# Optimization experiments

Hardware: AMD Instinct MI355X
Metric: run time of the kernel (lower is better)

The kernel has to match this reference:

```python
import jax, jax.numpy as jnp
import numpy as np

D_MODEL, N_HEADS, D_LLM = 1024, 16, 4096
D_KEYS = D_MODEL // N_HEADS  # 64


def setup_inputs() -> dict:
    key = jax.random.key(0)
    ks = jax.random.split(key, 11)
    s = lambda fan_in: 1.0 / np.sqrt(fan_in)
    inp = {
        "target_embedding": jax.random.normal(ks[0], (4, 2048, D_MODEL), jnp.float32),
        "source_embedding": jax.random.normal(ks[1], (4, 1024, D_LLM), jnp.float32),
        "value_embedding": jax.random.normal(ks[2], (4, 1024, D_LLM), jnp.float32),
        "Wq": jax.random.uniform(ks[3], (D_MODEL, D_KEYS * N_HEADS), jnp.float32, -s(D_MODEL), s(D_MODEL)),
        "bq": jax.random.uniform(ks[4], (D_KEYS * N_HEADS,), jnp.float32, -s(D_MODEL), s(D_MODEL)),
        "Wk": jax.random.uniform(ks[5], (D_LLM, D_KEYS * N_HEADS), jnp.float32, -s(D_LLM), s(D_LLM)),
        "bk": jax.random.uniform(ks[6], (D_KEYS * N_HEADS,), jnp.float32, -s(D_LLM), s(D_LLM)),
        "Wv": jax.random.uniform(ks[7], (D_LLM, D_KEYS * N_HEADS), jnp.float32, -s(D_LLM), s(D_LLM)),
        "bv": jax.random.uniform(ks[8], (D_KEYS * N_HEADS,), jnp.float32, -s(D_LLM), s(D_LLM)),
        "Wo": jax.random.uniform(ks[9], (D_KEYS * N_HEADS, D_MODEL), jnp.float32, -s(D_KEYS * N_HEADS), s(D_KEYS * N_HEADS)),
        "bo": jax.random.uniform(ks[10], (D_MODEL,), jnp.float32, -s(D_KEYS * N_HEADS), s(D_KEYS * N_HEADS)),
    }
    return inp


def reference(target_embedding, source_embedding, value_embedding,
              Wq, bq, Wk, bk, Wv, bv, Wo, bo):
    B, L, _ = target_embedding.shape
    _, S, _ = source_embedding.shape
    H, E = N_HEADS, D_KEYS
    q = (target_embedding @ Wq + bq).reshape(B, L, H, E)
    k = (source_embedding @ Wk + bk).reshape(B, S, H, E)
    v = (value_embedding @ Wv + bv).reshape(B, S, H, E)
    scale = 1.0 / np.sqrt(E)
    scores = jnp.einsum('blhe,bshe->bhls', q, k)  # [B,H,L,S]
    A = jax.nn.softmax(scale * scores, axis=-1)   # dropout = identity (eval mode)
    out = jnp.einsum('bhls,bshe->blhe', A, v).reshape(B, L, H * E)
    return out @ Wo + bo
```

## Files before the change

kernel.cpp:

```cpp
#include <hip/hip_runtime.h>
#include <hip/hip_bf16.h>

using bf16 = __hip_bfloat16;
typedef __attribute__((ext_vector_type(8))) short short8;
typedef __attribute__((ext_vector_type(4))) float f32x4;

static constexpr int Bc = 4, Lc = 2048, Sc = 1024;
static constexpr int DModel = 1024;

__device__ __forceinline__ void gload16(const void* g, void* l) {
  __builtin_amdgcn_global_load_lds((const __attribute__((address_space(1))) void*)g,
                                   (__attribute__((address_space(3))) void*)l,
                                   16, 0, 0);
}

__device__ __forceinline__ void wait_vm8()  { asm volatile("s_waitcnt vmcnt(8)" ::: "memory"); }
__device__ __forceinline__ void wait_vm4()  { asm volatile("s_waitcnt vmcnt(4)" ::: "memory"); }
__device__ __forceinline__ void wait_vm0()  { asm volatile("s_waitcnt vmcnt(0)" ::: "memory"); }
__device__ __forceinline__ void barrier_raw() { asm volatile("s_barrier" ::: "memory"); }

__global__ void cvt3(const float* __restrict__ a, bf16* __restrict__ ao, long na4,
                     const float* __restrict__ b, bf16* __restrict__ bo, long nb4,
                     const float* __restrict__ c, bf16* __restrict__ co, long nc4) {
  long total = na4 + nb4 + nc4;
  long stride = (long)gridDim.x * blockDim.x;
  for (long i = (long)blockIdx.x * blockDim.x + threadIdx.x; i < total; i += stride) {
    const float* src; bf16* dst; long j;
    if (i < na4)            { src = a; dst = ao; j = i; }
    else if (i < na4 + nb4) { src = b; dst = bo; j = i - na4; }
    else                    { src = c; dst = co; j = i - na4 - nb4; }
    float4 v = reinterpret_cast<const float4*>(src)[j];
    alignas(8) bf16 t[4] = {__float2bfloat16(v.x), __float2bfloat16(v.y),
                            __float2bfloat16(v.z), __float2bfloat16(v.w)};
    reinterpret_cast<ushort4*>(dst)[j] = *reinterpret_cast<const ushort4*>(t);
  }
}

__global__ __launch_bounds__(256) void transpose_cvt_w(const float* __restrict__ Wq, bf16* __restrict__ WqT,
                                                       const float* __restrict__ Wk, bf16* __restrict__ WkT,
                                                       const float* __restrict__ Wv, bf16* __restrict__ WvT,
                                                       const float* __restrict__ Wo, bf16* __restrict__ WoT) {
  __shared__ bf16 tile[32][33];
  int bid = blockIdx.x;
  const float* in; bf16* out; int R, l;
  if (bid < 1024)      { in = Wq; out = WqT; R = 1024; l = bid; }
  else if (bid < 5120) { in = Wk; out = WkT; R = 4096; l = bid - 1024; }
  else if (bid < 9216) { in = Wv; out = WvT; R = 4096; l = bid - 5120; }
  else                 { in = Wo; out = WoT; R = 1024; l = bid - 9216; }
  const int C = 1024;
  int bx = l & 31, by = l >> 5;
  int tx = threadIdx.x & 31, ty = threadIdx.x >> 5;
  int r0 = by * 32, c0 = bx * 32;
#pragma unroll
  for (int i = 0; i < 32; i += 8)
    tile[ty + i][tx] = __float2bfloat16(in[(long)(r0 + ty + i) * C + c0 + tx]);
  __syncthreads();
#pragma unroll
  for (int i = 0; i < 32; i += 8)
    out[(long)(c0 + ty + i) * R + r0 + tx] = tile[tx][ty + i];
}

__device__ __forceinline__ void gemm_core(const bf16* __restrict__ A, const bf16* __restrict__ Bt,
                                          const float* __restrict__ bias,
                                          bf16* __restrict__ Cb, float* __restrict__ Cf,
                                          bf16* __restrict__ Cvt,
                                          int N, int K, int bx, int by,
                                          bf16* As, bf16* Bs) {
  const int tid = threadIdx.x;
  const int lane = tid & 63, g = lane >> 4, lm = lane & 15;
  const int wid = tid >> 6, wr = wid >> 1, wc = wid & 1;
  const long brow = (long)by * 128, bcol = (long)bx * 128;

  const bf16* asrc[4];
  const bf16* bsrc[4];
  int dsto[4];
#pragma unroll
  for (int t = 0; t < 4; ++t) {
    int sl = tid + t * 256;
    int row = sl >> 3;
    int kg = (sl & 7) ^ (row & 7);
    asrc[t] = A + (brow + row) * (long)K + kg * 8;
    bsrc[t] = Bt + (bcol + row) * (long)K + kg * 8;
    dsto[t] = sl * 16;
  }

  f32x4 zero = {0.f, 0.f, 0.f, 0.f};
  f32x4 acc[4][4];
#pragma unroll
  for (int i = 0; i < 4; ++i)
#pragma unroll
    for (int j = 0; j < 4; ++j) acc[i][j] = zero;

  char* Asc = (char*)As;
  char* Bsc = (char*)Bs;

#pragma unroll
  for (int t = 0; t < 4; ++t) {
    gload16(asrc[t], Asc + dsto[t]);
    gload16(bsrc[t], Bsc + dsto[t]);
    asrc[t] += 64; bsrc[t] += 64;
  }

  const int nt = K >> 6;
  for (int i = 0; i < nt; ++i) {
    const int cur = i & 1;
    if (i + 1 < nt) {
      const int nxt = cur ^ 1;
#pragma unroll
      for (int t = 0; t < 4; ++t) {
        gload16(asrc[t], Asc + nxt * 16384 + dsto[t]);
        gload16(bsrc[t], Bsc + nxt * 16384 + dsto[t]);
        asrc[t] += 64; bsrc[t] += 64;
      }
      wait_vm8();
    } else {
      wait_vm0();
    }
    barrier_raw();

    const char* Ab = Asc + cur * 16384;
    const char* Bb = Bsc + cur * 16384;
    __builtin_amdgcn_s_setprio(1);
#pragma unroll
    for (int ks = 0; ks < 2; ++ks) {
      short8 af[4], bfv[4];
#pragma unroll
      for (int mi = 0; mi < 4; ++mi) {
        int m = wr * 64 + mi * 16 + lm;
        af[mi] = *reinterpret_cast<const short8*>(
            Ab + ((m * 128 + ks * 64 + g * 16) ^ ((m & 7) << 4)));
      }
#pragma unroll
      for (int ni = 0; ni < 4; ++ni) {
        int n = wc * 64 + ni * 16 + lm;
        bfv[ni] = *reinterpret_cast<const short8*>(
            Bb + ((n * 128 + ks * 64 + g * 16) ^ ((n & 7) << 4)));
      }
#pragma unroll
      for (int mi = 0; mi < 4; ++mi)
#pragma unroll
        for (int ni = 0; ni < 4; ++ni)
          acc[mi][ni] = __builtin_amdgcn_mfma_f32_16x16x32_bf16(af[mi], bfv[ni], acc[mi][ni], 0, 0, 0);
    }
    __builtin_amdgcn_s_setprio(0);
    barrier_raw();
  }

#pragma unroll
  for (int ni = 0; ni < 4; ++ni) {
    long n = bcol + wc * 64 + ni * 16 + lm;
    float bv = bias ? bias[n] : 0.f;
#pragma unroll
    for (int mi = 0; mi < 4; ++mi) {
      long m0 = brow + wr * 64 + mi * 16 + g * 4;
      if (Cvt) {
        long b = m0 >> 10, s0 = m0 & 1023;
        alignas(8) bf16 t4[4];
#pragma unroll
        for (int r = 0; r < 4; ++r) t4[r] = __float2bfloat16(acc[mi][ni][r] + bv);
        *reinterpret_cast<ushort4*>(Cvt + ((b << 10) + n) * 1024 + s0) =
            *reinterpret_cast<const ushort4*>(t4);
      } else {
#pragma unroll
        for (int r = 0; r < 4; ++r) {
          float o = acc[mi][ni][r] + bv;
          if (Cb) Cb[(m0 + r) * N + n] = __float2bfloat16(o);
          else    Cf[(m0 + r) * N + n] = o;
        }
      }
    }
  }
}

__global__ __launch_bounds__(256) void gemm_bt(const bf16* __restrict__ A,
                                               const bf16* __restrict__ Bt,
                                               const float* __restrict__ bias,
                                               bf16* __restrict__ Cb,
                                               float* __restrict__ Cf,
                                               int N, int K) {
  __shared__ bf16 As[2 * 128 * 64];
  __shared__ bf16 Bs[2 * 128 * 64];
  int bid = blockIdx.x;
  int g = (bid & 7) * (gridDim.x >> 3) + (bid >> 3);
  gemm_core(A, Bt, bias, Cb, Cf, nullptr, N, K, g & 7, g >> 3, As, Bs);
}

__global__ __launch_bounds__(256) void gemm_qkv(
    const bf16* __restrict__ Ak, const bf16* __restrict__ Bk, const float* __restrict__ bk_, bf16* __restrict__ Ck, int Kk, int nbk,
    const bf16* __restrict__ Av, const bf16* __restrict__ Bv_, const float* __restrict__ bv_, bf16* __restrict__ CvT, int Kv, int nbv,
    const bf16* __restrict__ Aq, const bf16* __restrict__ Bq_, const float* __restrict__ bq_, bf16* __restrict__ Cq, int Kq) {
  __shared__ bf16 As[2 * 128 * 64];
  __shared__ bf16 Bs[2 * 128 * 64];
  int bid = blockIdx.x;
  const bf16 *A, *Bt; const float* bias; bf16 *C = nullptr, *Cvt = nullptr; int K, l, nb;
  if (bid < nbk)            { A = Ak; Bt = Bk;  bias = bk_; C = Ck;    K = Kk; l = bid;             nb = nbk; }
  else if (bid < nbk + nbv) { A = Av; Bt = Bv_; bias = bv_; Cvt = CvT; K = Kv; l = bid - nbk;       nb = nbv; }
  else                      { A = Aq; Bt = Bq_; bias = bq_; C = Cq;   K = Kq; l = bid - nbk - nbv; nb = gridDim.x - nbk - nbv; }
  int g = (l & 7) * (nb >> 3) + (l >> 3);
  gemm_core(A, Bt, bias, C, nullptr, Cvt, 1024, K, g & 7, g >> 3, As, Bs);
}

__global__ __launch_bounds__(256) void attn_fused(const bf16* __restrict__ q,
                                                  const bf16* __restrict__ k,
                                                  const bf16* __restrict__ vT,
                                                  bf16* __restrict__ o) {
  constexpr float C2 = 0.18033688011112042f;
  constexpr float THR = 6.0f;
  __shared__ bf16 Kl[2][64 * 64];
  __shared__ bf16 Vl[2][64 * 64];
  __shared__ bf16 Pl[4][16 * 64];
  const int tid = threadIdx.x;
  const int lane = tid & 63, g = lane >> 4, lm = lane & 15;
  const int wid = tid >> 6;
  int bid = blockIdx.x;
  int gl = (bid & 7) * 256 + (bid >> 3);
  const int qt = gl & 31, bh = gl >> 5;
  const int b = bh >> 4, h = bh & 15;
  const int qbase = qt * 64 + wid * 16;

  const bf16* qrow = q + (long)(b * Lc + qbase + lm) * DModel + h * 64;
  short8 qa0 = *reinterpret_cast<const short8*>(qrow + g * 8);
  short8 qa1 = *reinterpret_cast<const short8*>(qrow + 32 + g * 8);
#pragma unroll
  for (int j = 0; j < 8; ++j) {
    union { ushort u; bf16 h; } cv;
    cv.u = (ushort)qa0[j];
    bf16 s0 = __float2bfloat16(__bfloat162float(cv.h) * C2);
    qa0[j] = (short)*reinterpret_cast<ushort*>(&s0);
    cv.u = (ushort)qa1[j];
    bf16 s1 = __float2bfloat16(__bfloat162float(cv.h) * C2);
    qa1[j] = (short)*reinterpret_cast<ushort*>(&s1);
  }

  const bf16* kbase = k + (long)b * Sc * DModel + h * 64;
  const bf16* vbase = vT + ((long)b * DModel + h * 64) * Sc;

  const bf16* ksrc[2];
  const bf16* vsrc[2];
  int dsto[2];
#pragma unroll
  for (int t = 0; t < 2; ++t) {
    int sl = tid + t * 256;
    int row = sl >> 3;
    int cg = (sl & 7) ^ (row & 7);
    ksrc[t] = kbase + (long)row * DModel + cg * 8;
    vsrc[t] = vbase + (long)row * Sc + cg * 8;
    dsto[t] = sl * 16;
  }

  f32x4 zero = {0.f, 0.f, 0.f, 0.f};
  f32x4 accO[4];
#pragma unroll
  for (int i = 0; i < 4; ++i) accO[i] = zero;
  f32x4 accL = zero;
  float mst[4] = {-1e30f, -1e30f, -1e30f, -1e30f};

  short8 vones;
#pragma unroll
  for (int j = 0; j < 8; ++j) vones[j] = (short)0x3F80;

  char* Klc = (char*)Kl;
  char* Vlc = (char*)Vl;
  char* Plc = (char*)Pl + wid * (16 * 64 * 2);

#pragma unroll
  for (int t = 0; t < 2; ++t) {
    gload16(ksrc[t], Klc + dsto[t]);
    gload16(vsrc[t], Vlc + dsto[t]);
    ksrc[t] += 64 * DModel; vsrc[t] += 64;
  }

  for (int j = 0; j < Sc / 64; ++j) {
    const int cur = j & 1;
    if (j + 1 < Sc / 64) {
      const int nxt = cur ^ 1;
#pragma unroll
      for (int t = 0; t < 2; ++t) {
        gload16(ksrc[t], Klc + nxt * 8192 + dsto[t]);
        gload16(vsrc[t], Vlc + nxt * 8192 + dsto[t]);
        ksrc[t] += 64 * DModel; vsrc[t] += 64;
      }
      wait_vm4();
    } else {
      wait_vm0();
    }
    barrier_raw();

    const char* Kb = Klc + cur * 8192;
    const char* Vb = Vlc + cur * 8192;

    f32x4 scv[4];
    __builtin_amdgcn_s_setprio(1);
#pragma unroll
    for (int st = 0; st < 4; ++st) {
      int s = st * 16 + lm;
      int sw = (s & 7) << 4;
      short8 kb0 = *reinterpret_cast<const short8*>(Kb + ((s * 128 + g * 16) ^ sw));
      short8 kb1 = *reinterpret_cast<const short8*>(Kb + ((s * 128 + 64 + g * 16) ^ sw));
      f32x4 z = zero;
      z = __builtin_amdgcn_mfma_f32_16x16x32_bf16(qa0, kb0, z, 0, 0, 0);
      z = __builtin_amdgcn_mfma_f32_16x16x32_bf16(qa1, kb1, z, 0, 0, 0);
      scv[st] = z;
    }
    __builtin_amdgcn_s_setprio(0);

    float pmax[4];
#pragma unroll
    for (int r = 0; r < 4; ++r)
      pmax[r] = fmaxf(fmaxf(scv[0][r], scv[1][r]), fmaxf(scv[2][r], scv[3][r]));
    int need = 0;
#pragma unroll
    for (int r = 0; r < 4; ++r) need |= (pmax[r] > mst[r] + THR) ? 1 : 0;
    if (__any(need)) {
#pragma unroll
      for (int r = 0; r < 4; ++r) {
        float mx = pmax[r];
        mx = fmaxf(mx, __shfl_xor(mx, 1));
        mx = fmaxf(mx, __shfl_xor(mx, 2));
        mx = fmaxf(mx, __shfl_xor(mx, 4));
        mx = fmaxf(mx, __shfl_xor(mx, 8));
        float mnew = fmaxf(mst[r], mx);
        float corr = __builtin_amdgcn_exp2f(mst[r] - mnew);
        mst[r] = mnew;
        accL[r] *= corr;
#pragma unroll
        for (int et = 0; et < 4; ++et) accO[et][r] *= corr;
      }
    }
#pragma unroll
    for (int r = 0; r < 4; ++r) {
      int qq = g * 4 + r;
      int swp = (qq & 7) << 4;
#pragma unroll
      for (int st = 0; st < 4; ++st) {
        float p = __builtin_amdgcn_exp2f(scv[st][r] - mst[r]);
        *reinterpret_cast<bf16*>(Plc + ((qq * 128 + (st * 16 + lm) * 2) ^ swp)) =
            __float2bfloat16(p);
      }
    }

    __builtin_amdgcn_s_setprio(1);
#pragma unroll
    for (int sk = 0; sk < 2; ++sk) {
      short8 pa = *reinterpret_cast<const short8*>(
          Plc + ((lm * 128 + sk * 64 + g * 16) ^ ((lm & 7) << 4)));
      accL = __builtin_amdgcn_mfma_f32_16x16x32_bf16(pa, vones, accL, 0, 0, 0);
#pragma unroll
      for (int et = 0; et < 4; ++et) {
        int e = et * 16 + lm;
        short8 vb = *reinterpret_cast<const short8*>(
            Vb + ((e * 128 + sk * 64 + g * 16) ^ ((e & 7) << 4)));
        accO[et] = __builtin_amdgcn_mfma_f32_16x16x32_bf16(pa, vb, accO[et], 0, 0, 0);
      }
    }
    __builtin_amdgcn_s_setprio(0);
    barrier_raw();
  }

#pragma unroll
  for (int r = 0; r < 4; ++r) {
    float inv = 1.0f / accL[r];
    long row = (long)(b * Lc + qbase + g * 4 + r);
#pragma unroll
    for (int et = 0; et < 4; ++et)
      o[row * DModel + h * 64 + et * 16 + lm] = __float2bfloat16(accO[et][r] * inv);
  }
}

extern "C" void kernel_launch(void* const* d_in, const int* in_sizes, int n_in,
                              void* d_out, int out_size, void* d_ws, size_t ws_size,
                              hipStream_t stream) {
  const float* tgt = (const float*)d_in[0];
  const float* src = (const float*)d_in[1];
  const float* val = (const float*)d_in[2];
  const float* Wq  = (const float*)d_in[3];
  const float* bq  = (const float*)d_in[4];
  const float* Wk  = (const float*)d_in[5];
  const float* bk  = (const float*)d_in[6];
  const float* Wv  = (const float*)d_in[7];
  const float* bv  = (const float*)d_in[8];
  const float* Wo  = (const float*)d_in[9];
  const float* bo  = (const float*)d_in[10];
  float* out = (float*)d_out;
  char* ws = (char*)d_ws;

  const long n4_tgt = (long)8192 * 1024 / 4;
  const long n4_sv  = (long)4096 * 4096 / 4;

  if (ws_size < (132ul << 20)) return;

  bf16* WqT  = (bf16*)(ws + (0l   << 20));
  bf16* WkT  = (bf16*)(ws + (2l   << 20));
  bf16* WvT  = (bf16*)(ws + (10l  << 20));
  bf16* WoT  = (bf16*)(ws + (18l  << 20));
  bf16* tgtb = (bf16*)(ws + (20l  << 20));
  bf16* srcb = (bf16*)(ws + (36l  << 20));
  bf16* valb = (bf16*)(ws + (68l  << 20));
  bf16* qb   = (bf16*)(ws + (100l << 20));
  bf16* kb   = (bf16*)(ws + (116l << 20));
  bf16* vTb  = (bf16*)(ws + (124l << 20));
  bf16* attnb = tgtb;

  transpose_cvt_w<<<10240, 256, 0, stream>>>(Wq, WqT, Wk, WkT, Wv, WvT, Wo, WoT);
  cvt3<<<4096, 256, 0, stream>>>(tgt, tgtb, n4_tgt, src, srcb, n4_sv, val, valb, n4_sv);
  gemm_qkv<<<1024, 256, 0, stream>>>(srcb, WkT, bk, kb, 4096, 256,
                                     valb, WvT, bv, vTb, 4096, 256,
                                     tgtb, WqT, bq, qb, 1024);
  attn_fused<<<2048, 256, 0, stream>>>(qb, kb, vTb, attnb);
  gemm_bt<<<512, 256, 0, stream>>>(attnb, WoT, bo, (bf16*)nullptr, out, 1024, 1024);
}
```

Before: 252.5 us.

## Use 256x256 tiles with 4-stage pipeline for fused QKV projection GEMM

Replaces the 128x128 QKV projection GEMM with a 512-thread kernel computing 256x256 output tiles. It uses a four-stage global-to-LDS pipeline with BK=32 and staged vmcnt waits, plus a new swizzle. Larger tiles cut global/L2 traffic per FLOP and keep more loads in flight. In exchange the grid drops to 256 blocks, about one per CU, and Q blocks (K=1024) finish far earlier than K/V blocks, so load imbalance and register pressure are risks.

```diff
diff --git a/kernel.cpp b/kernel.cpp
--- a/kernel.cpp
+++ b/kernel.cpp
@@ -14,6 +14,7 @@
                                    16, 0, 0);
 }
 
+__device__ __forceinline__ void wait_vm12() { asm volatile("s_waitcnt vmcnt(12)" ::: "memory"); }
 __device__ __forceinline__ void wait_vm8()  { asm volatile("s_waitcnt vmcnt(8)" ::: "memory"); }
 __device__ __forceinline__ void wait_vm4()  { asm volatile("s_waitcnt vmcnt(4)" ::: "memory"); }
 __device__ __forceinline__ void wait_vm0()  { asm volatile("s_waitcnt vmcnt(0)" ::: "memory"); }
@@ -60,10 +61,133 @@
     out[(long)(c0 + ty + i) * R + r0 + tx] = tile[tx][ty + i];
 }
 
+__device__ __forceinline__ void gemm256_core(const bf16* __restrict__ A, const bf16* __restrict__ Bt,
+                                             const float* __restrict__ bias,
+                                             bf16* __restrict__ Cb, float* __restrict__ Cf,
+                                             bf16* __restrict__ Cvt,
+                                             int N, int K, int bx, int by,
+                                             bf16* lds) {
+  const int tid = threadIdx.x;
+  const int lane = tid & 63, g = lane >> 4, lm = lane & 15;
+  const int wid = tid >> 6, wr = wid >> 2, wc = wid & 3;
+  const long brow = (long)by * 256, bcol = (long)bx * 256;
+
+  char* Asc = (char*)lds;
+  char* Bsc = (char*)(lds + 4 * 8192);
+
+  const bf16* asrc[2];
+  const bf16* bsrc[2];
+  int dsto[2];
+#pragma unroll
+  for (int t = 0; t < 2; ++t) {
+    int sl = tid + t * 512;
+    int row = sl >> 2;
+    int ks = (sl & 3) ^ ((row >> 1) & 3);
+    asrc[t] = A + (brow + row) * (long)K + ks * 8;
+    bsrc[t] = Bt + (bcol + row) * (long)K + ks * 8;
+    dsto[t] = sl * 16;
+  }
+
+#define STAGE256(buf)                                        \
+  {                                                          \
+    const int _bo = (buf) * 16384;                           \
+    _Pragma("unroll")                                        \
+    for (int _t = 0; _t < 2; ++_t) {                         \
+      gload16(asrc[_t], Asc + _bo + dsto[_t]);               \
+      gload16(bsrc[_t], Bsc + _bo + dsto[_t]);               \
+      asrc[_t] += 32; bsrc[_t] += 32;                        \
+    }                                                        \
+  }
+
+  f32x4 zero = {0.f, 0.f, 0.f, 0.f};
+  f32x4 acc[8][4];
+#pragma unroll
+  for (int i = 0; i < 8; ++i)
+#pragma unroll
+    for (int j = 0; j < 4; ++j) acc[i][j] = zero;
+
+  STAGE256(0);
+  STAGE256(1);
+  STAGE256(2);
+
+  const int nt = K >> 5;
+  for (int t = 0; t < nt; ++t) {
+    const int rem = nt - 1 - t;
+    if (rem >= 3) { STAGE256((t + 3) & 3); wait_vm12(); }
+    else if (rem == 2) wait_vm8();
+    else if (rem == 1) wait_vm4();
+    else               wait_vm0();
+    barrier_raw();
+
+    const char* Ab = Asc + (t & 3) * 16384;
+    const char* Bb = Bsc + (t & 3) * 16384;
+    short8 af[8], bfv[4];
+#pragma unroll
+    for (int mi = 0; mi < 8; ++mi) {
+      int row = wr * 128 + mi * 16 + lm;
+      af[mi] = *reinterpret_cast<const short8*>(
+          Ab + row * 64 + ((g ^ ((row >> 1) & 3)) << 4));
+    }
+#pragma unroll
+    for (int ni = 0; ni < 4; ++ni) {
+      int row = wc * 64 + ni * 16 + lm;
+      bfv[ni] = *reinterpret_cast<const short8*>(
+          Bb + row * 64 + ((g ^ ((row >> 1) & 3)) << 4));
+    }
+    __builtin_amdgcn_s_setprio(1);
+#pragma unroll
+    for (int mi = 0; mi < 8; ++mi)
+#pragma unroll
+      for (int ni = 0; ni < 4; ++ni)
+        acc[mi][ni] = __builtin_amdgcn_mfma_f32_16x16x32_bf16(af[mi], bfv[ni], acc[mi][ni], 0, 0, 0);
+    __builtin_amdgcn_s_setprio(0);
+    barrier_raw();
+  }
+#undef STAGE256
+
+#pragma unroll
+  for (int ni = 0; ni < 4; ++ni) {
+    long n = bcol + wc * 64 + ni * 16 + lm;
+    float bv = bias ? bias[n] : 0.f;
+#pragma unroll
+    for (int mi = 0; mi < 8; ++mi) {
+      long m0 = brow + wr * 128 + mi * 16 + g * 4;
+      if (Cvt) {
+        long b = m0 >> 10, s0 = m0 & 1023;
+        alignas(8) bf16 t4[4];
+#pragma unroll
+        for (int r = 0; r < 4; ++r) t4[r] = __float2bfloat16(acc[mi][ni][r] + bv);
+        *reinterpret_cast<ushort4*>(Cvt + ((b << 10) + n) * 1024 + s0) =
+            *reinterpret_cast<const ushort4*>(t4);
+      } else {
+#pragma unroll
+        for (int r = 0; r < 4; ++r) {
+          float o = acc[mi][ni][r] + bv;
+          if (Cb) Cb[(m0 + r) * N + n] = __float2bfloat16(o);
+          else    Cf[(m0 + r) * N + n] = o;
+        }
+      }
+    }
+  }
+}
+
+__global__ __launch_bounds__(512, 2) void gemm_qkv256(
+    const bf16* __restrict__ Ak, const bf16* __restrict__ Bk, const float* __restrict__ bk_, bf16* __restrict__ Ck, int Kk, int nbk,
+    const bf16* __restrict__ Av, const bf16* __restrict__ Bv_, const float* __restrict__ bv_, bf16* __restrict__ CvT, int Kv, int nbv,
+    const bf16* __restrict__ Aq, const bf16* __restrict__ Bq_, const float* __restrict__ bq_, bf16* __restrict__ Cq, int Kq) {
+  __shared__ bf16 lds[8 * 8192];
+  int bid = blockIdx.x;
+  const bf16 *A, *Bt; const float* bias; bf16 *C = nullptr, *Cvt = nullptr; int K, l, nb;
+  if (bid < nbk)            { A = Ak; Bt = Bk;  bias = bk_; C = Ck;    K = Kk; l = bid;             nb = nbk; }
+  else if (bid < nbk + nbv) { A = Av; Bt = Bv_; bias = bv_; Cvt = CvT; K = Kv; l = bid - nbk;       nb = nbv; }
+  else                      { A = Aq; Bt = Bq_; bias = bq_; C = Cq;   K = Kq; l = bid - nbk - nbv; nb = gridDim.x - nbk - nbv; }
+  int g = (l & 7) * (nb >> 3) + (l >> 3);
+  gemm256_core(A, Bt, bias, C, nullptr, Cvt, 1024, K, g & 3, g >> 2, lds);
+}
+
 __device__ __forceinline__ void gemm_core(const bf16* __restrict__ A, const bf16* __restrict__ Bt,
                                           const float* __restrict__ bias,
                                           bf16* __restrict__ Cb, float* __restrict__ Cf,
-                                          bf16* __restrict__ Cvt,
                                           int N, int K, int bx, int by,
                                           bf16* As, bf16* Bs) {
   const int tid = threadIdx.x;
@@ -153,20 +277,11 @@
 #pragma unroll
     for (int mi = 0; mi < 4; ++mi) {
       long m0 = brow + wr * 64 + mi * 16 + g * 4;
-      if (Cvt) {
-        long b = m0 >> 10, s0 = m0 & 1023;
-        alignas(8) bf16 t4[4];
-#pragma unroll
-        for (int r = 0; r < 4; ++r) t4[r] = __float2bfloat16(acc[mi][ni][r] + bv);
-        *reinterpret_cast<ushort4*>(Cvt + ((b << 10) + n) * 1024 + s0) =
-            *reinterpret_cast<const ushort4*>(t4);
-      } else {
-#pragma unroll
-        for (int r = 0; r < 4; ++r) {
-          float o = acc[mi][ni][r] + bv;
-          if (Cb) Cb[(m0 + r) * N + n] = __float2bfloat16(o);
-          else    Cf[(m0 + r) * N + n] = o;
-        }
+#pragma unroll
+      for (int r = 0; r < 4; ++r) {
+        float o = acc[mi][ni][r] + bv;
+        if (Cb) Cb[(m0 + r) * N + n] = __float2bfloat16(o);
+        else    Cf[(m0 + r) * N + n] = o;
       }
     }
   }
@@ -182,22 +297,7 @@
   __shared__ bf16 Bs[2 * 128 * 64];
   int bid = blockIdx.x;
   int g = (bid & 7) * (gridDim.x >> 3) + (bid >> 3);
-  gemm_core(A, Bt, bias, Cb, Cf, nullptr, N, K, g & 7, g >> 3, As, Bs);
-}
-
-__global__ __launch_bounds__(256) void gemm_qkv(
-    const bf16* __restrict__ Ak, const bf16* __restrict__ Bk, const float* __restrict__ bk_, bf16* __restrict__ Ck, int Kk, int nbk,
-    const bf16* __restrict__ Av, const bf16* __restrict__ Bv_, const float* __restrict__ bv_, bf16* __restrict__ CvT, int Kv, int nbv,
-    const bf16* __restrict__ Aq, const bf16* __restrict__ Bq_, const float* __restrict__ bq_, bf16* __restrict__ Cq, int Kq) {
-  __shared__ bf16 As[2 * 128 * 64];
-  __shared__ bf16 Bs[2 * 128 * 64];
-  int bid = blockIdx.x;
-  const bf16 *A, *Bt; const float* bias; bf16 *C = nullptr, *Cvt = nullptr; int K, l, nb;
-  if (bid < nbk)            { A = Ak; Bt = Bk;  bias = bk_; C = Ck;    K = Kk; l = bid;             nb = nbk; }
-  else if (bid < nbk + nbv) { A = Av; Bt = Bv_; bias = bv_; Cvt = CvT; K = Kv; l = bid - nbk;       nb = nbv; }
-  else                      { A = Aq; Bt = Bq_; bias = bq_; C = Cq;   K = Kq; l = bid - nbk - nbv; nb = gridDim.x - nbk - nbv; }
-  int g = (l & 7) * (nb >> 3) + (l >> 3);
-  gemm_core(A, Bt, bias, C, nullptr, Cvt, 1024, K, g & 7, g >> 3, As, Bs);
+  gemm_core(A, Bt, bias, Cb, Cf, N, K, g & 7, g >> 3, As, Bs);
 }
 
 __global__ __launch_bounds__(256) void attn_fused(const bf16* __restrict__ q,
@@ -403,9 +503,9 @@
 
   transpose_cvt_w<<<10240, 256, 0, stream>>>(Wq, WqT, Wk, WkT, Wv, WvT, Wo, WoT);
   cvt3<<<4096, 256, 0, stream>>>(tgt, tgtb, n4_tgt, src, srcb, n4_sv, val, valb, n4_sv);
-  gemm_qkv<<<1024, 256, 0, stream>>>(srcb, WkT, bk, kb, 4096, 256,
-                                     valb, WvT, bv, vTb, 4096, 256,
-                                     tgtb, WqT, bq, qb, 1024);
+  gemm_qkv256<<<256, 512, 0, stream>>>(srcb, WkT, bk, kb, 4096, 64,
+                                       valb, WvT, bv, vTb, 4096, 64,
+                                       tgtb, WqT, bq, qb, 1024);
   attn_fused<<<2048, 256, 0, stream>>>(qb, kb, vTb, attnb);
   gemm_bt<<<512, 256, 0, stream>>>(attnb, WoT, bo, (bf16*)nullptr, out, 1024, 1024);
 }
```

Result: slower. 275.9 us (+9.2%).

## Replace QKV projection GEMM with 256x256-tile 8-wave ping-pong kernel

Applied to the files above, without the earlier changes.

The fused QKV projection GEMM now uses 256x256 output tiles with 512 threads (8 waves) and 128KB of LDS. Loads are staged in 128-row halves interleaved with four MFMA phases per K step, so global-to-LDS copies overlap with compute. Larger tiles raise arithmetic intensity and cut global traffic per FLOP. In exchange the grid shrinks to 256 blocks, which may underfill the device's CUs, and register pressure rises from the 32 accumulators per thread.

```diff
diff --git a/kernel.cpp b/kernel.cpp
--- a/kernel.cpp
+++ b/kernel.cpp
@@ -16,6 +16,7 @@
 
 __device__ __forceinline__ void wait_vm8()  { asm volatile("s_waitcnt vmcnt(8)" ::: "memory"); }
 __device__ __forceinline__ void wait_vm4()  { asm volatile("s_waitcnt vmcnt(4)" ::: "memory"); }
+__device__ __forceinline__ void wait_vm2()  { asm volatile("s_waitcnt vmcnt(2)" ::: "memory"); }
 __device__ __forceinline__ void wait_vm0()  { asm volatile("s_waitcnt vmcnt(0)" ::: "memory"); }
 __device__ __forceinline__ void barrier_raw() { asm volatile("s_barrier" ::: "memory"); }
 
@@ -60,10 +61,156 @@
     out[(long)(c0 + ty + i) * R + r0 + tx] = tile[tx][ty + i];
 }
 
+__device__ __forceinline__ void gemm8p_core(const bf16* __restrict__ A, const bf16* __restrict__ Bt,
+                                            const float* __restrict__ bias,
+                                            bf16* __restrict__ Cb, float* __restrict__ Cf,
+                                            bf16* __restrict__ Cvt,
+                                            int N, int K, int bx, int by,
+                                            bf16* lds) {
+  const int tid = threadIdx.x;
+  const int lane = tid & 63, g = lane >> 4, lm = lane & 15;
+  const int wid = tid >> 6, wr = wid >> 2, wc = wid & 3;
+  const long brow = (long)by * 256, bcol = (long)bx * 256;
+
+  char* Al = (char*)lds;
+  char* Bl = (char*)lds + 65536;
+
+  const int row0 = tid >> 3,          kg0 = (tid & 7) ^ (row0 & 7);
+  const int row1 = (tid + 512) >> 3,  kg1 = ((tid + 512) & 7) ^ (row1 & 7);
+  const int d0 = tid * 16, d1 = (tid + 512) * 16;
+  const bf16* aS0 = A + (brow + row0) * (long)K + kg0 * 8;
+  const bf16* aS1 = A + (brow + row1) * (long)K + kg1 * 8;
+  const bf16* bS0 = Bt + (bcol + row0) * (long)K + kg0 * 8;
+  const bf16* bS1 = Bt + (bcol + row1) * (long)K + kg1 * 8;
+  const long hK = 128l * K;
+
+#define STAGE_A(t_, h_) { const long so_ = (long)(h_) * hK + (long)(t_) * 64;  \
+    const int bo_ = (((t_) & 1) * 2 + (h_)) * 16384;                            \
+    gload16(aS0 + so_, Al + bo_ + d0); gload16(aS1 + so_, Al + bo_ + d1); }
+#define STAGE_B(t_, h_) { const long so_ = (long)(h_) * hK + (long)(t_) * 64;  \
+    const int bo_ = (((t_) & 1) * 2 + (h_)) * 16384;                            \
+    gload16(bS0 + so_, Bl + bo_ + d0); gload16(bS1 + so_, Bl + bo_ + d1); }
+
+#define LDA(qm_)                                                                \
+  _Pragma("unroll") for (int mi = 0; mi < 4; ++mi)                              \
+  _Pragma("unroll") for (int ks = 0; ks < 2; ++ks) {                            \
+    const int r_ = wr * 64 + mi * 16 + lm;                                      \
+    aR[mi][ks] = *reinterpret_cast<const short8*>(                              \
+        Al + (buf * 2 + (qm_)) * 16384 + r_ * 128 +                             \
+        ((((ks << 2) + g) ^ (r_ & 7)) << 4)); }
+#define LDB(qn_)                                                                \
+  _Pragma("unroll") for (int ni = 0; ni < 2; ++ni)                              \
+  _Pragma("unroll") for (int ks = 0; ks < 2; ++ks) {                            \
+    const int r_ = wc * 32 + ni * 16 + lm;                                      \
+    bR[ni][ks] = *reinterpret_cast<const short8*>(                              \
+        Bl + (buf * 2 + (qn_)) * 16384 + r_ * 128 +                             \
+        ((((ks << 2) + g) ^ (r_ & 7)) << 4)); }
+#define PHASE_MFMA(f_)                                                          \
+  __builtin_amdgcn_s_setprio(1);                                                \
+  _Pragma("unroll") for (int mi = 0; mi < 4; ++mi)                              \
+  _Pragma("unroll") for (int ni = 0; ni < 2; ++ni)                              \
+  _Pragma("unroll") for (int ks = 0; ks < 2; ++ks)                              \
+    acc[f_][mi][ni] = __builtin_amdgcn_mfma_f32_16x16x32_bf16(                  \
+        aR[mi][ks], bR[ni][ks], acc[f_][mi][ni], 0, 0, 0);                      \
+  __builtin_amdgcn_s_setprio(0);
+
+  f32x4 zero = {0.f, 0.f, 0.f, 0.f};
+  f32x4 acc[4][4][2];
+#pragma unroll
+  for (int f = 0; f < 4; ++f)
+#pragma unroll
+    for (int i = 0; i < 4; ++i)
+#pragma unroll
+      for (int j = 0; j < 2; ++j) acc[f][i][j] = zero;
+
+  short8 aR[4][2], bR[2][2];
+
+  STAGE_A(0, 0); STAGE_B(0, 0); STAGE_B(0, 1); STAGE_A(0, 1);
+  wait_vm4();
+  barrier_raw();
+
+  const int nt = K >> 6;
+  for (int t = 0; t < nt; ++t) {
+    const int buf = t & 1;
+    const bool more = (t + 1 < nt);
+    LDA(0); LDB(0);
+    if (more) STAGE_A(t + 1, 0);
+    barrier_raw();
+    PHASE_MFMA(0);
+    if (more) wait_vm4(); else wait_vm2();
+    barrier_raw();
+    LDB(1);
+    if (more) STAGE_B(t + 1, 0);
+    barrier_raw();
+    PHASE_MFMA(1);
+    if (more) wait_vm4(); else wait_vm0();
+    barrier_raw();
+    LDA(1);
+    if (more) STAGE_B(t + 1, 1);
+    barrier_raw();
+    PHASE_MFMA(2);
+    barrier_raw();
+    LDB(0);
+    if (more) STAGE_A(t + 1, 1);
+    barrier_raw();
+    PHASE_MFMA(3);
+    if (more) wait_vm4();
+    barrier_raw();
+  }
+#undef STAGE_A
+#undef STAGE_B
+#undef LDA
+#undef LDB
+#undef PHASE_MFMA
+
+  const int QMv[4] = {0, 0, 1, 1}, QNv[4] = {0, 1, 1, 0};
+#pragma unroll
+  for (int f = 0; f < 4; ++f) {
+    const int qm = QMv[f], qn = QNv[f];
+#pragma unroll
+    for (int ni = 0; ni < 2; ++ni) {
+      long n = bcol + qn * 128 + wc * 32 + ni * 16 + lm;
+      float bv = bias ? bias[n] : 0.f;
+#pragma unroll
+      for (int mi = 0; mi < 4; ++mi) {
+        long m0 = brow + qm * 128 + wr * 64 + mi * 16 + g * 4;
+        if (Cvt) {
+          long b = m0 >> 10, s0 = m0 & 1023;
+          alignas(8) bf16 t4[4];
+#pragma unroll
+          for (int r = 0; r < 4; ++r) t4[r] = __float2bfloat16(acc[f][mi][ni][r] + bv);
+          *reinterpret_cast<ushort4*>(Cvt + ((b << 10) + n) * 1024 + s0) =
+              *reinterpret_cast<const ushort4*>(t4);
+        } else {
+#pragma unroll
+          for (int r = 0; r < 4; ++r) {
+            float o = acc[f][mi][ni][r] + bv;
+            if (Cb) Cb[(m0 + r) * N + n] = __float2bfloat16(o);
+            else    Cf[(m0 + r) * N + n] = o;
+          }
+        }
+      }
+    }
+  }
+}
+
+__global__ __launch_bounds__(512, 2) void gemm_qkv8p(
+    const bf16* __restrict__ Ak, const bf16* __restrict__ Bk, const float* __restrict__ bk_, bf16* __restrict__ Ck, int Kk, int nbk,
+    const bf16* __restrict__ Av, const bf16* __restrict__ Bv_, const float* __restrict__ bv_, bf16* __restrict__ CvT, int Kv, int nbv,
+    const bf16* __restrict__ Aq, const bf16* __restrict__ Bq_, const float* __restrict__ bq_, bf16* __restrict__ Cq, int Kq) {
+  __shared__ bf16 lds[65536];
+  int bid = blockIdx.x;
+  const bf16 *A, *Bt; const float* bias; bf16 *C = nullptr, *Cvt = nullptr; int K, l, nb;
+  if (bid < nbk)            { A = Ak; Bt = Bk;  bias = bk_; C = Ck;    K = Kk; l = bid;             nb = nbk; }
+  else if (bid < nbk + nbv) { A = Av; Bt = Bv_; bias = bv_; Cvt = CvT; K = Kv; l = bid - nbk;       nb = nbv; }
+  else                      { A = Aq; Bt = Bq_; bias = bq_; C = Cq;   K = Kq; l = bid - nbk - nbv; nb = gridDim.x - nbk - nbv; }
+  int g = (l & 7) * (nb >> 3) + (l >> 3);
+  gemm8p_core(A, Bt, bias, C, nullptr, Cvt, 1024, K, g & 3, g >> 2, lds);
+}
+
 __device__ __forceinline__ void gemm_core(const bf16* __restrict__ A, const bf16* __restrict__ Bt,
                                           const float* __restrict__ bias,
                                           bf16* __restrict__ Cb, float* __restrict__ Cf,
-                                          bf16* __restrict__ Cvt,
                                           int N, int K, int bx, int by,
                                           bf16* As, bf16* Bs) {
   const int tid = threadIdx.x;
@@ -153,20 +300,11 @@
 #pragma unroll
     for (int mi = 0; mi < 4; ++mi) {
       long m0 = brow + wr * 64 + mi * 16 + g * 4;
-      if (Cvt) {
-        long b = m0 >> 10, s0 = m0 & 1023;
-        alignas(8) bf16 t4[4];
-#pragma unroll
-        for (int r = 0; r < 4; ++r) t4[r] = __float2bfloat16(acc[mi][ni][r] + bv);
-        *reinterpret_cast<ushort4*>(Cvt + ((b << 10) + n) * 1024 + s0) =
-            *reinterpret_cast<const ushort4*>(t4);
-      } else {
-#pragma unroll
-        for (int r = 0; r < 4; ++r) {
-          float o = acc[mi][ni][r] + bv;
-          if (Cb) Cb[(m0 + r) * N + n] = __float2bfloat16(o);
-          else    Cf[(m0 + r) * N + n] = o;
-        }
+#pragma unroll
+      for (int r = 0; r < 4; ++r) {
+        float o = acc[mi][ni][r] + bv;
+        if (Cb) Cb[(m0 + r) * N + n] = __float2bfloat16(o);
+        else    Cf[(m0 + r) * N + n] = o;
       }
     }
   }
@@ -182,22 +320,7 @@
   __shared__ bf16 Bs[2 * 128 * 64];
   int bid = blockIdx.x;
   int g = (bid & 7) * (gridDim.x >> 3) + (bid >> 3);
-  gemm_core(A, Bt, bias, Cb, Cf, nullptr, N, K, g & 7, g >> 3, As, Bs);
-}
-
-__global__ __launch_bounds__(256) void gemm_qkv(
-    const bf16* __restrict__ Ak, const bf16* __restrict__ Bk, const float* __restrict__ bk_, bf16* __restrict__ Ck, int Kk, int nbk,
-    const bf16* __restrict__ Av, const bf16* __restrict__ Bv_, const float* __restrict__ bv_, bf16* __restrict__ CvT, int Kv, int nbv,
-    const bf16* __restrict__ Aq, const bf16* __restrict__ Bq_, const float* __restrict__ bq_, bf16* __restrict__ Cq, int Kq) {
-  __shared__ bf16 As[2 * 128 * 64];
-  __shared__ bf16 Bs[2 * 128 * 64];
-  int bid = blockIdx.x;
-  const bf16 *A, *Bt; const float* bias; bf16 *C = nullptr, *Cvt = nullptr; int K, l, nb;
-  if (bid < nbk)            { A = Ak; Bt = Bk;  bias = bk_; C = Ck;    K = Kk; l = bid;             nb = nbk; }
-  else if (bid < nbk + nbv) { A = Av; Bt = Bv_; bias = bv_; Cvt = CvT; K = Kv; l = bid - nbk;       nb = nbv; }
-  else                      { A = Aq; Bt = Bq_; bias = bq_; C = Cq;   K = Kq; l = bid - nbk - nbv; nb = gridDim.x - nbk - nbv; }
-  int g = (l & 7) * (nb >> 3) + (l >> 3);
-  gemm_core(A, Bt, bias, C, nullptr, Cvt, 1024, K, g & 7, g >> 3, As, Bs);
+  gemm_core(A, Bt, bias, Cb, Cf, N, K, g & 7, g >> 3, As, Bs);
 }
 
 __global__ __launch_bounds__(256) void attn_fused(const bf16* __restrict__ q,
@@ -403,9 +526,9 @@
 
   transpose_cvt_w<<<10240, 256, 0, stream>>>(Wq, WqT, Wk, WkT, Wv, WvT, Wo, WoT);
   cvt3<<<4096, 256, 0, stream>>>(tgt, tgtb, n4_tgt, src, srcb, n4_sv, val, valb, n4_sv);
-  gemm_qkv<<<1024, 256, 0, stream>>>(srcb, WkT, bk, kb, 4096, 256,
-                                     valb, WvT, bv, vTb, 4096, 256,
-                                     tgtb, WqT, bq, qb, 1024);
+  gemm_qkv8p<<<256, 512, 0, stream>>>(srcb, WkT, bk, kb, 4096, 64,
+                                      valb, WvT, bv, vTb, 4096, 64,
+                                      tgtb, WqT, bq, qb, 1024);
   attn_fused<<<2048, 256, 0, stream>>>(qb, kb, vTb, attnb);
   gemm_bt<<<512, 256, 0, stream>>>(attnb, WoT, bo, (bf16*)nullptr, out, 1024, 1024);
 }
```

Result: slower. 269.7 us (+6.8%).
